# Performance work log

Hardware: AMD Instinct MI355X
Metric: run time of the kernel (lower is better)

The kernel has to match this reference:

```python
import jax, jax.numpy as jnp
import numpy as np

HEADS = 8
DIM = 64      # dim
DH = 64       # dim_head
DK = 24       # dim_k (== dim_head_k * heads, required by reshape in forward)
DHK = 3       # dim_head_k (also conv groups)


def setup_inputs() -> dict:
    key = jax.random.key(0)
    ks = jax.random.split(key, 10)
    b, h, w = 4, 128, 128
    return {
        "x_in": jax.random.normal(ks[0], (b, h, w, DIM), jnp.float32),
        "illu_fea_trans": jax.random.normal(ks[1], (b, h, w, DIM), jnp.float32),
        "illu_map_trans": jax.random.normal(ks[2], (b, h, w, DK), jnp.float32),
        # Linear weights stored as [in, out] (torch stores [out, in]; math y = x @ W_in_out)
        "Wq": jax.random.normal(ks[3], (DIM, HEADS * DH), jnp.float32) * 0.05,
        "Wk": jax.random.normal(ks[4], (DK, HEADS * DHK), jnp.float32) * 0.05,
        "Wv": jax.random.normal(ks[5], (DIM, HEADS * DH), jnp.float32) * 0.05,
        "rescale": jnp.ones((HEADS, 1, 1), jnp.float32),
        "Wp": jax.random.normal(ks[6], (HEADS * DHK, DK), jnp.float32) * 0.05,
        "bp": jax.random.normal(ks[7], (DK,), jnp.float32) * 0.05,
        # grouped conv weights, OIHW: [out=24, in/groups=8, 3, 3]
        "conv1_w": jax.random.normal(ks[8], (DK, DK // DHK, 3, 3), jnp.float32) * 0.05,
        "conv2_w": jax.random.normal(ks[9], (DK, DK // DHK, 3, 3), jnp.float32) * 0.05,
    }


def _gconv(x_nchw, w_oihw):
    return jax.lax.conv_general_dilated(
        x_nchw, w_oihw, window_strides=(1, 1), padding='SAME',
        feature_group_count=DHK,
        dimension_numbers=('NCHW', 'OIHW', 'NCHW'))


def reference(x_in, illu_fea_trans, illu_map_trans, Wq, Wk, Wv, rescale, Wp, bp, conv1_w, conv2_w):
    b, h, w, c = x_in.shape
    n = h * w
    # projections
    q = (x_in.reshape(b, n, c) @ Wq).reshape(b, n, HEADS, DH)
    k_inp = illu_map_trans.reshape(b, n, DK) @ Wk            # [b, n, heads*dhk]
    v = (illu_fea_trans.reshape(b, n, c) @ Wv).reshape(b, n, HEADS, DH)
    kh = k_inp.reshape(b, n, HEADS, DHK)
    q = q / (DIM ** 0.5)  # note: scaled by sqrt(dim), not sqrt(dim_head)
    # channel-wise cross-attention: attn over channel dims, contracting tokens n
    attn = jnp.einsum('bnhk,bnhd->bhkd', kh, q) * rescale[None]  # [b, heads, dhk, dh]
    attn = jax.nn.softmax(attn, axis=-1)
    out = jnp.einsum('bhkd,bnhd->bnkh', attn, v)             # [b, n, dhk, heads]
    out = out.reshape(b, n, DHK * HEADS) @ Wp + bp           # proj
    out = out.reshape(b, h, w, DK)
    # positional branch: two grouped 3x3 convs with exact GELU on k_inp
    kx = k_inp.reshape(b, h, w, DK).transpose(0, 3, 1, 2)    # NCHW
    y = _gconv(kx, conv1_w)
    y = jax.nn.gelu(y, approximate=False)
    y = _gconv(y, conv2_w)
    return out + y.transpose(0, 2, 3, 1)
```

## Files before the change

### kernel.cpp

```cpp
#include <hip/hip_runtime.h>
#include <math.h>

#define HEADS 8
#define DIM   64
#define DK    24
#define DHK   3
#define BB    4
#define HH    128
#define WW    128
#define NN    (HH*WW)
#define QSCALE 0.125f

__global__ __launch_bounds__(256) void s_reduce_kproj(
    const float* __restrict__ imap,
    const float* __restrict__ x,
    const float* __restrict__ Wk,
    float* __restrict__ k_inp,
    float* __restrict__ Sp_part)
{
    __shared__ float lds[4*1536];
    const int tid = threadIdx.x;
    const int blk = blockIdx.x;
    const int b = blk >> 7, chunk = blk & 127;
    const int w = tid >> 6, lane = tid & 63;
    const int cq = lane & 15;
    const int ig = lane >> 4;

    const long tokB = (long)b * NN + chunk * 128;
    const long tok0 = tokB + w * 32;
    const float* xp = x    + tok0 * 64 + cq * 4;
    const float* mp = imap + tok0 * 24 + ig * 6;

    float acc[6][4];
    #pragma unroll
    for (int r = 0; r < 6; ++r)
        #pragma unroll
        for (int q = 0; q < 4; ++q) acc[r][q] = 0.f;

    for (int t = 0; t < 32; ++t) {
        float4 xv = *(const float4*)(xp + t * 64);
        float2 m0 = *(const float2*)(mp + t * 24);
        float2 m1 = *(const float2*)(mp + t * 24 + 2);
        float2 m2 = *(const float2*)(mp + t * 24 + 4);
        float mm[6] = {m0.x, m0.y, m1.x, m1.y, m2.x, m2.y};
        #pragma unroll
        for (int r = 0; r < 6; ++r) {
            acc[r][0] += mm[r] * xv.x;
            acc[r][1] += mm[r] * xv.y;
            acc[r][2] += mm[r] * xv.z;
            acc[r][3] += mm[r] * xv.w;
        }
    }

    float* pp = lds + w * 1536;
    #pragma unroll
    for (int r = 0; r < 6; ++r) {
        float4 v = {acc[r][0], acc[r][1], acc[r][2], acc[r][3]};
        *(float4*)(pp + (ig * 6 + r) * 64 + cq * 4) = v;
    }
    __syncthreads();

    for (int e = tid; e < 1536; e += 256)
        Sp_part[(long)blk * 1536 + e] =
            lds[e] + lds[1536 + e] + lds[3072 + e] + lds[4608 + e];

    float kv[24];
    if (tid < 128) {
        const float4* m4 = (const float4*)(imap + (tokB + tid) * 24);
        float m[24];
        #pragma unroll
        for (int i = 0; i < 6; ++i) {
            float4 v = m4[i];
            m[4*i+0]=v.x; m[4*i+1]=v.y; m[4*i+2]=v.z; m[4*i+3]=v.w;
        }
        #pragma unroll
        for (int j = 0; j < 24; ++j) kv[j] = 0.f;
        for (int i = 0; i < 24; ++i) {
            float mi = m[i];
            #pragma unroll
            for (int j = 0; j < 24; ++j) kv[j] += mi * Wk[i * 24 + j];
        }
    }
    __syncthreads();
    if (tid < 128) {
        #pragma unroll
        for (int j = 0; j < 24; ++j) lds[tid * 25 + j] = kv[j];
    }
    __syncthreads();
    for (int e = tid; e < 128 * 24; e += 256)
        k_inp[tokB * 24 + e] = lds[(e / 24) * 25 + (e % 24)];
}

__global__ __launch_bounds__(256) void sp_reduce(
    const float* __restrict__ Sp_part, float* __restrict__ Sp)
{
    const int blk = blockIdx.x;
    const int b = blk / 6, eb = blk % 6;
    const int e = eb * 256 + threadIdx.x;
    const float* p = Sp_part + (long)b * 128 * 1536 + e;
    float s0 = 0.f, s1 = 0.f, s2 = 0.f, s3 = 0.f;
    for (int c = 0; c < 128; c += 4) {
        s0 += p[(long)(c + 0) * 1536];
        s1 += p[(long)(c + 1) * 1536];
        s2 += p[(long)(c + 2) * 1536];
        s3 += p[(long)(c + 3) * 1536];
    }
    Sp[b * 1536 + e] = (s0 + s1) + (s2 + s3);
}

__global__ __launch_bounds__(256) void attn_p(
    const float* __restrict__ Sp,
    const float* __restrict__ Wk,
    const float* __restrict__ Wq,
    const float* __restrict__ Wv,
    const float* __restrict__ rescale,
    const float* __restrict__ Wp,
    float* __restrict__ Pt)
{
    __shared__ float Sp_l[1536];
    __shared__ float S_l[1536];
    __shared__ float att[1536];
    __shared__ float M_l[1536];

    const int b = blockIdx.x, tid = threadIdx.x;

    for (int i = tid; i < 1536; i += 256) Sp_l[i] = Sp[b * 1536 + i];
    __syncthreads();

    for (int q = tid; q < 1536; q += 256) {
        int c = q & 63, j = q >> 6;
        float s = 0.f;
        #pragma unroll
        for (int i = 0; i < 24; ++i) s += Wk[i * 24 + j] * Sp_l[i * 64 + c];
        S_l[q] = s;
    }
    __syncthreads();

    for (int q = tid; q < 1536; q += 256) {
        int d = q & 63, ch = q >> 6;
        int h = ch / 3;
        const float* wq = Wq + h * 64 + d;
        const float* sr = S_l + ch * 64;
        float s = 0.f;
        for (int cc = 0; cc < 64; ++cc) s += sr[cc] * wq[cc * 512];
        att[q] = s * QSCALE * rescale[h];
    }
    __syncthreads();

    if (tid < 24) {
        float* row = att + tid * 64;
        float mx = row[0];
        for (int d = 1; d < 64; ++d) mx = fmaxf(mx, row[d]);
        float sum = 0.f;
        for (int d = 0; d < 64; ++d) { float e = expf(row[d] - mx); row[d] = e; sum += e; }
        float inv = 1.f / sum;
        for (int d = 0; d < 64; ++d) row[d] *= inv;
    }
    __syncthreads();

    for (int q = tid; q < 1536; q += 256) {
        int c = q & 63, ch = q >> 6;
        int h = ch / 3;
        const float* wv = Wv + c * 512 + h * 64;
        const float* ar = att + ch * 64;
        float s = 0.f;
        for (int d = 0; d < 64; ++d) s += ar[d] * wv[d];
        M_l[ch * 64 + c] = s;
    }
    __syncthreads();

    for (int q = tid; q < 1536; q += 256) {
        int c = q & 63, jo = q >> 6;
        float s = 0.f;
        #pragma unroll
        for (int k = 0; k < 3; ++k)
            #pragma unroll
            for (int h = 0; h < 8; ++h)
                s += M_l[(h * 3 + k) * 64 + c] * Wp[(k * 8 + h) * 24 + jo];
        Pt[b * 1536 + q] = s;
    }
}

#define CONV_PROLOG(CWPTR)                                                    \
    const int tid = threadIdx.x;                                              \
    const int o = tid % 24, jj = tid / 24;                                    \
    const int blk = blockIdx.x;                                               \
    const int b = blk >> 8, ti = (blk >> 4) & 15, tj = blk & 15;              \
    const int i0 = ti * 8, j0 = tj * 8;                                       \
    const int g = o >> 3;                                                     \
    float wr[8][9];                                                           \
    {                                                                         \
        const float4* wp = (const float4*)((CWPTR) + o * 72);                 \
        _Pragma("unroll")                                                     \
        for (int t = 0; t < 18; ++t) ((float4*)wr)[t] = wp[t];                \
    }                                                                         \
    const int gj0 = j0 + jj - 1;                                              \
    const bool cok0 = gj0 >= 0;                                               \
    const bool cok2 = (j0 + jj + 1) < WW;

#define LOADROW(IN, GI, SLOT)                                                 \
    {                                                                         \
        const int gi_ = (GI);                                                 \
        const bool rok_ = (gi_ >= 0) & (gi_ < HH);                            \
        const float* rp_ = (IN) + (long)b * NN * 24 + g * 8                   \
                         + ((long)gi_ * WW + gj0) * 24;                       \
        float4 z_ = {0.f,0.f,0.f,0.f};                                        \
        float4 a0_=z_, a1_=z_, b0_=z_, b1_=z_, c0_=z_, c1_=z_;                \
        if (rok_ & cok0) { a0_ = *(const float4*)(rp_);                       \
                           a1_ = *(const float4*)(rp_ + 4); }                 \
        if (rok_)        { b0_ = *(const float4*)(rp_ + 24);                  \
                           b1_ = *(const float4*)(rp_ + 28); }                \
        if (rok_ & cok2) { c0_ = *(const float4*)(rp_ + 48);                  \
                           c1_ = *(const float4*)(rp_ + 52); }                \
        *(float4*)&win[SLOT][0][0] = a0_; *(float4*)&win[SLOT][0][4] = a1_;   \
        *(float4*)&win[SLOT][1][0] = b0_; *(float4*)&win[SLOT][1][4] = b1_;   \
        *(float4*)&win[SLOT][2][0] = c0_; *(float4*)&win[SLOT][2][4] = c1_;   \
    }

__global__ __launch_bounds__(192, 2) void conv1_gelu(
    const float* __restrict__ kin, const float* __restrict__ cw,
    float* __restrict__ y1)
{
    CONV_PROLOG(cw)
    float win[3][3][8];
    LOADROW(kin, i0 - 1, 0)
    LOADROW(kin, i0,     1)
    #pragma unroll
    for (int ii = 0; ii < 8; ++ii) {
        LOADROW(kin, i0 + ii + 1, (ii + 2) % 3)
        float s = 0.f;
        #pragma unroll
        for (int di = 0; di < 3; ++di) {
            const int slot = (ii + di) % 3;
            #pragma unroll
            for (int dj = 0; dj < 3; ++dj)
                #pragma unroll
                for (int ic = 0; ic < 8; ++ic)
                    s += win[slot][dj][ic] * wr[ic][di * 3 + dj];
        }
        s = 0.5f * s * (1.f + erff(s * 0.70710678f));
        y1[((long)((b * HH + i0 + ii) * WW + j0)) * 24 + tid] = s;
    }
}

__global__ __launch_bounds__(192, 2) void conv2_proj(
    const float* __restrict__ y1, const float* __restrict__ fea,
    const float* __restrict__ cw2, const float* __restrict__ Pt,
    const float* __restrict__ bp, float* __restrict__ outp)
{
    CONV_PROLOG(cw2)

    float acc[8];
    {
        const float bo = bp[o];
        #pragma unroll
        for (int ii = 0; ii < 8; ++ii) acc[ii] = bo;
        const float* PtRow = Pt + b * 1536 + o * 64;
        const float* feaB = fea + (((long)(b * HH + i0)) * WW + (j0 + jj)) * 64;
        for (int cq = 0; cq < 16; ++cq) {
            float4 p = *(const float4*)(PtRow + cq * 4);
            #pragma unroll
            for (int ii = 0; ii < 8; ++ii) {
                float4 f = *(const float4*)(feaB + (long)ii * WW * 64 + cq * 4);
                acc[ii] += f.x * p.x + f.y * p.y + f.z * p.z + f.w * p.w;
            }
        }
    }

    float win[3][3][8];
    LOADROW(y1, i0 - 1, 0)
    LOADROW(y1, i0,     1)
    #pragma unroll
    for (int ii = 0; ii < 8; ++ii) {
        LOADROW(y1, i0 + ii + 1, (ii + 2) % 3)
        float s = 0.f;
        #pragma unroll
        for (int di = 0; di < 3; ++di) {
            const int slot = (ii + di) % 3;
            #pragma unroll
            for (int dj = 0; dj < 3; ++dj)
                #pragma unroll
                for (int ic = 0; ic < 8; ++ic)
                    s += win[slot][dj][ic] * wr[ic][di * 3 + dj];
        }
        outp[((long)((b * HH + i0 + ii) * WW + j0)) * 24 + tid] = acc[ii] + s;
    }
}

extern "C" void kernel_launch(void* const* d_in, const int* in_sizes, int n_in,
                              void* d_out, int out_size, void* d_ws, size_t ws_size,
                              hipStream_t stream) {
    const float* x_in    = (const float*)d_in[0];
    const float* fea     = (const float*)d_in[1];
    const float* imap    = (const float*)d_in[2];
    const float* Wq      = (const float*)d_in[3];
    const float* Wk      = (const float*)d_in[4];
    const float* Wv      = (const float*)d_in[5];
    const float* rescale = (const float*)d_in[6];
    const float* Wp      = (const float*)d_in[7];
    const float* bp      = (const float*)d_in[8];
    const float* c1w     = (const float*)d_in[9];
    const float* c2w     = (const float*)d_in[10];
    float* out = (float*)d_out;

    float* ws      = (float*)d_ws;
    float* k_inp   = ws;
    float* y1      = ws + 1572864;
    float* Sp_part = ws + 3145728;
    float* Sp      = ws + 3932160;
    float* Pt      = ws + 3938304;

    s_reduce_kproj<<<512, 256, 0, stream>>>(imap, x_in, Wk, k_inp, Sp_part);
    sp_reduce<<<24, 256, 0, stream>>>(Sp_part, Sp);
    attn_p<<<4, 256, 0, stream>>>(Sp, Wk, Wq, Wv, rescale, Wp, Pt);
    conv1_gelu<<<BB * 256, 192, 0, stream>>>(k_inp, c1w, y1);
    conv2_proj<<<BB * 256, 192, 0, stream>>>(y1, fea, c2w, Pt, bp, out);
}
```

Baseline: 178.8 us.

## Fuse k projection into conv1 via LDS halo tile and fold Sp reduction into attention

Computes the Wk projection of illu_map directly inside the first conv kernel for a 10x10 halo tile in shared memory, eliminating the k_inp global buffer write and reread. The separate Sp partial-reduction kernel is removed and its summation moved into the 4-block attention kernel. This cuts one launch and global traffic, at the cost of redundant halo projection work and a less parallel reduction running on only four blocks.

```diff
diff --git a/kernel.cpp b/kernel.cpp
--- a/kernel.cpp
+++ b/kernel.cpp
@@ -11,14 +11,12 @@
 #define NN    (HH*WW)
 #define QSCALE 0.125f
 
-__global__ __launch_bounds__(256) void s_reduce_kproj(
+__global__ __launch_bounds__(256) void s_reduce(
     const float* __restrict__ imap,
     const float* __restrict__ x,
-    const float* __restrict__ Wk,
-    float* __restrict__ k_inp,
     float* __restrict__ Sp_part)
 {
-    __shared__ float lds[4*1536];
+    __shared__ float part[4*1536];
     const int tid = threadIdx.x;
     const int blk = blockIdx.x;
     const int b = blk >> 7, chunk = blk & 127;
@@ -26,8 +24,7 @@
     const int cq = lane & 15;
     const int ig = lane >> 4;
 
-    const long tokB = (long)b * NN + chunk * 128;
-    const long tok0 = tokB + w * 32;
+    const long tok0 = (long)b * NN + chunk * 128 + w * 32;
     const float* xp = x    + tok0 * 64 + cq * 4;
     const float* mp = imap + tok0 * 24 + ig * 6;
 
@@ -52,7 +49,7 @@
         }
     }
 
-    float* pp = lds + w * 1536;
+    float* pp = part + w * 1536;
     #pragma unroll
     for (int r = 0; r < 6; ++r) {
         float4 v = {acc[r][0], acc[r][1], acc[r][2], acc[r][3]};
@@ -62,54 +59,11 @@
 
     for (int e = tid; e < 1536; e += 256)
         Sp_part[(long)blk * 1536 + e] =
-            lds[e] + lds[1536 + e] + lds[3072 + e] + lds[4608 + e];
-
-    float kv[24];
-    if (tid < 128) {
-        const float4* m4 = (const float4*)(imap + (tokB + tid) * 24);
-        float m[24];
-        #pragma unroll
-        for (int i = 0; i < 6; ++i) {
-            float4 v = m4[i];
-            m[4*i+0]=v.x; m[4*i+1]=v.y; m[4*i+2]=v.z; m[4*i+3]=v.w;
-        }
-        #pragma unroll
-        for (int j = 0; j < 24; ++j) kv[j] = 0.f;
-        for (int i = 0; i < 24; ++i) {
-            float mi = m[i];
-            #pragma unroll
-            for (int j = 0; j < 24; ++j) kv[j] += mi * Wk[i * 24 + j];
-        }
-    }
-    __syncthreads();
-    if (tid < 128) {
-        #pragma unroll
-        for (int j = 0; j < 24; ++j) lds[tid * 25 + j] = kv[j];
-    }
-    __syncthreads();
-    for (int e = tid; e < 128 * 24; e += 256)
-        k_inp[tokB * 24 + e] = lds[(e / 24) * 25 + (e % 24)];
-}
-
-__global__ __launch_bounds__(256) void sp_reduce(
-    const float* __restrict__ Sp_part, float* __restrict__ Sp)
-{
-    const int blk = blockIdx.x;
-    const int b = blk / 6, eb = blk % 6;
-    const int e = eb * 256 + threadIdx.x;
-    const float* p = Sp_part + (long)b * 128 * 1536 + e;
-    float s0 = 0.f, s1 = 0.f, s2 = 0.f, s3 = 0.f;
-    for (int c = 0; c < 128; c += 4) {
-        s0 += p[(long)(c + 0) * 1536];
-        s1 += p[(long)(c + 1) * 1536];
-        s2 += p[(long)(c + 2) * 1536];
-        s3 += p[(long)(c + 3) * 1536];
-    }
-    Sp[b * 1536 + e] = (s0 + s1) + (s2 + s3);
-}
-
-__global__ __launch_bounds__(256) void attn_p(
-    const float* __restrict__ Sp,
+            part[e] + part[1536 + e] + part[3072 + e] + part[4608 + e];
+}
+
+__global__ __launch_bounds__(256) void attn_fused(
+    const float* __restrict__ Sp_part,
     const float* __restrict__ Wk,
     const float* __restrict__ Wq,
     const float* __restrict__ Wv,
@@ -124,7 +78,17 @@
 
     const int b = blockIdx.x, tid = threadIdx.x;
 
-    for (int i = tid; i < 1536; i += 256) Sp_l[i] = Sp[b * 1536 + i];
+    {
+        float s[6] = {0.f, 0.f, 0.f, 0.f, 0.f, 0.f};
+        const float* p = Sp_part + (long)b * 128 * 1536;
+        for (int c = 0; c < 128; ++c) {
+            #pragma unroll
+            for (int k = 0; k < 6; ++k)
+                s[k] += p[(long)c * 1536 + tid + 256 * k];
+        }
+        #pragma unroll
+        for (int k = 0; k < 6; ++k) Sp_l[tid + 256 * k] = s[k];
+    }
     __syncthreads();
 
     for (int q = tid; q < 1536; q += 256) {
@@ -181,28 +145,130 @@
     }
 }
 
-#define CONV_PROLOG(CWPTR)                                                    \
-    const int tid = threadIdx.x;                                              \
-    const int o = tid % 24, jj = tid / 24;                                    \
-    const int blk = blockIdx.x;                                               \
-    const int b = blk >> 8, ti = (blk >> 4) & 15, tj = blk & 15;              \
-    const int i0 = ti * 8, j0 = tj * 8;                                       \
-    const int g = o >> 3;                                                     \
-    float wr[8][9];                                                           \
+__global__ __launch_bounds__(192, 2) void conv1_kproj_gelu(
+    const float* __restrict__ imap, const float* __restrict__ Wk,
+    const float* __restrict__ cw, float* __restrict__ y1)
+{
+    __shared__ __align__(16) float kbuf[100 * 28];
+
+    const int tid = threadIdx.x;
+    const int blk = blockIdx.x;
+    const int b = blk >> 8, ti = (blk >> 4) & 15, tj = blk & 15;
+    const int i0 = ti * 8, j0 = tj * 8;
+
+    if (tid < 100) {
+        const int pi = tid / 10, pj = tid % 10;
+        const int gi = i0 + pi - 1, gj = j0 + pj - 1;
+        float kv[24];
+        #pragma unroll
+        for (int j = 0; j < 24; ++j) kv[j] = 0.f;
+        if (gi >= 0 && gi < HH && gj >= 0 && gj < WW) {
+            const float4* m4 = (const float4*)(imap + (((long)b * HH + gi) * WW + gj) * 24);
+            float m[24];
+            #pragma unroll
+            for (int i = 0; i < 6; ++i) {
+                float4 v = m4[i];
+                m[4*i+0]=v.x; m[4*i+1]=v.y; m[4*i+2]=v.z; m[4*i+3]=v.w;
+            }
+            for (int i = 0; i < 24; ++i) {
+                float mi = m[i];
+                #pragma unroll
+                for (int j = 0; j < 24; ++j) kv[j] += mi * Wk[i * 24 + j];
+            }
+        }
+        #pragma unroll
+        for (int j = 0; j < 24; ++j) kbuf[tid * 28 + j] = kv[j];
+    }
+    __syncthreads();
+
+    const int o = tid % 24, jj = tid / 24;
+    const int g = o >> 3;
+
+    float wr[8][9];
+    {
+        const float4* wp = (const float4*)(cw + o * 72);
+        #pragma unroll
+        for (int t = 0; t < 18; ++t) ((float4*)wr)[t] = wp[t];
+    }
+
+    float win[3][3][8];
+    #define LROW(R, SLOT)                                                     \
     {                                                                         \
-        const float4* wp = (const float4*)((CWPTR) + o * 72);                 \
-        _Pragma("unroll")                                                     \
-        for (int t = 0; t < 18; ++t) ((float4*)wr)[t] = wp[t];                \
-    }                                                                         \
-    const int gj0 = j0 + jj - 1;                                              \
-    const bool cok0 = gj0 >= 0;                                               \
+        const float* rp_ = kbuf + ((R) * 10 + jj) * 28 + g * 8;               \
+        *(float4*)&win[SLOT][0][0] = *(const float4*)(rp_);                   \
+        *(float4*)&win[SLOT][0][4] = *(const float4*)(rp_ + 4);               \
+        *(float4*)&win[SLOT][1][0] = *(const float4*)(rp_ + 28);              \
+        *(float4*)&win[SLOT][1][4] = *(const float4*)(rp_ + 32);              \
+        *(float4*)&win[SLOT][2][0] = *(const float4*)(rp_ + 56);              \
+        *(float4*)&win[SLOT][2][4] = *(const float4*)(rp_ + 60);              \
+    }
+
+    LROW(0, 0)
+    LROW(1, 1)
+    #pragma unroll
+    for (int ii = 0; ii < 8; ++ii) {
+        LROW(ii + 2, (ii + 2) % 3)
+        float s = 0.f;
+        #pragma unroll
+        for (int di = 0; di < 3; ++di) {
+            const int slot = (ii + di) % 3;
+            #pragma unroll
+            for (int dj = 0; dj < 3; ++dj)
+                #pragma unroll
+                for (int ic = 0; ic < 8; ++ic)
+                    s += win[slot][dj][ic] * wr[ic][di * 3 + dj];
+        }
+        s = 0.5f * s * (1.f + erff(s * 0.70710678f));
+        y1[((long)((b * HH + i0 + ii) * WW + j0)) * 24 + tid] = s;
+    }
+    #undef LROW
+}
+
+__global__ __launch_bounds__(192, 2) void conv2_proj(
+    const float* __restrict__ y1, const float* __restrict__ fea,
+    const float* __restrict__ cw2, const float* __restrict__ Pt,
+    const float* __restrict__ bp, float* __restrict__ outp)
+{
+    const int tid = threadIdx.x;
+    const int o = tid % 24, jj = tid / 24;
+    const int blk = blockIdx.x;
+    const int b = blk >> 8, ti = (blk >> 4) & 15, tj = blk & 15;
+    const int i0 = ti * 8, j0 = tj * 8;
+    const int g = o >> 3;
+
+    float wr[8][9];
+    {
+        const float4* wp = (const float4*)(cw2 + o * 72);
+        #pragma unroll
+        for (int t = 0; t < 18; ++t) ((float4*)wr)[t] = wp[t];
+    }
+    const int gj0 = j0 + jj - 1;
+    const bool cok0 = gj0 >= 0;
     const bool cok2 = (j0 + jj + 1) < WW;
 
-#define LOADROW(IN, GI, SLOT)                                                 \
+    float acc[8];
+    {
+        const float bo = bp[o];
+        #pragma unroll
+        for (int ii = 0; ii < 8; ++ii) acc[ii] = bo;
+        const float* PtRow = Pt + b * 1536 + o * 64;
+        const float* feaB = fea + (((long)(b * HH + i0)) * WW + (j0 + jj)) * 64;
+        for (int cq = 0; cq < 16; ++cq) {
+            float4 p = *(const float4*)(PtRow + cq * 4);
+            #pragma unroll
+            for (int ii = 0; ii < 8; ++ii) {
+                float4 f = *(const float4*)(feaB + (long)ii * WW * 64 + cq * 4);
+                acc[ii] += f.x * p.x + f.y * p.y + f.z * p.z + f.w * p.w;
+            }
+        }
+    }
+
+    float win[3][3][8];
+    #define LOADROW(GI, SLOT)                                                 \
     {                                                                         \
         const int gi_ = (GI);                                                 \
         const bool rok_ = (gi_ >= 0) & (gi_ < HH);                            \
-        const float* rp_ = (IN) + (long)b * NN * 24 + g * 8                   \
+        const float* rp_ = y1 + (long)b * NN * 24 + g * 8                     \
                          + ((long)gi_ * WW + gj0) * 24;                       \
         float4 z_ = {0.f,0.f,0.f,0.f};                                        \
         float4 a0_=z_, a1_=z_, b0_=z_, b1_=z_, c0_=z_, c1_=z_;                \
@@ -217,17 +283,11 @@
         *(float4*)&win[SLOT][2][0] = c0_; *(float4*)&win[SLOT][2][4] = c1_;   \
     }
 
-__global__ __launch_bounds__(192, 2) void conv1_gelu(
-    const float* __restrict__ kin, const float* __restrict__ cw,
-    float* __restrict__ y1)
-{
-    CONV_PROLOG(cw)
-    float win[3][3][8];
-    LOADROW(kin, i0 - 1, 0)
-    LOADROW(kin, i0,     1)
+    LOADROW(i0 - 1, 0)
+    LOADROW(i0,     1)
     #pragma unroll
     for (int ii = 0; ii < 8; ++ii) {
-        LOADROW(kin, i0 + ii + 1, (ii + 2) % 3)
+        LOADROW(i0 + ii + 1, (ii + 2) % 3)
         float s = 0.f;
         #pragma unroll
         for (int di = 0; di < 3; ++di) {
@@ -238,53 +298,9 @@
                 for (int ic = 0; ic < 8; ++ic)
                     s += win[slot][dj][ic] * wr[ic][di * 3 + dj];
         }
-        s = 0.5f * s * (1.f + erff(s * 0.70710678f));
-        y1[((long)((b * HH + i0 + ii) * WW + j0)) * 24 + tid] = s;
-    }
-}
-
-__global__ __launch_bounds__(192, 2) void conv2_proj(
-    const float* __restrict__ y1, const float* __restrict__ fea,
-    const float* __restrict__ cw2, const float* __restrict__ Pt,
-    const float* __restrict__ bp, float* __restrict__ outp)
-{
-    CONV_PROLOG(cw2)
-
-    float acc[8];
-    {
-        const float bo = bp[o];
-        #pragma unroll
-        for (int ii = 0; ii < 8; ++ii) acc[ii] = bo;
-        const float* PtRow = Pt + b * 1536 + o * 64;
-        const float* feaB = fea + (((long)(b * HH + i0)) * WW + (j0 + jj)) * 64;
-        for (int cq = 0; cq < 16; ++cq) {
-            float4 p = *(const float4*)(PtRow + cq * 4);
-            #pragma unroll
-            for (int ii = 0; ii < 8; ++ii) {
-                float4 f = *(const float4*)(feaB + (long)ii * WW * 64 + cq * 4);
-                acc[ii] += f.x * p.x + f.y * p.y + f.z * p.z + f.w * p.w;
-            }
-        }
-    }
-
-    float win[3][3][8];
-    LOADROW(y1, i0 - 1, 0)
-    LOADROW(y1, i0,     1)
-    #pragma unroll
-    for (int ii = 0; ii < 8; ++ii) {
-        LOADROW(y1, i0 + ii + 1, (ii + 2) % 3)
-        float s = 0.f;
-        #pragma unroll
-        for (int di = 0; di < 3; ++di) {
-            const int slot = (ii + di) % 3;
-            #pragma unroll
-            for (int dj = 0; dj < 3; ++dj)
-                #pragma unroll
-                for (int ic = 0; ic < 8; ++ic)
-                    s += win[slot][dj][ic] * wr[ic][di * 3 + dj];
-        }
         outp[((long)((b * HH + i0 + ii) * WW + j0)) * 24 + tid] = acc[ii] + s;
     }
+    #undef LOADROW
 }
 
 extern "C" void kernel_launch(void* const* d_in, const int* in_sizes, int n_in,
@@ -304,15 +320,12 @@
     float* out = (float*)d_out;
 
     float* ws      = (float*)d_ws;
-    float* k_inp   = ws;
-    float* y1      = ws + 1572864;
-    float* Sp_part = ws + 3145728;
-    float* Sp      = ws + 3932160;
-    float* Pt      = ws + 3938304;
-
-    s_reduce_kproj<<<512, 256, 0, stream>>>(imap, x_in, Wk, k_inp, Sp_part);
-    sp_reduce<<<24, 256, 0, stream>>>(Sp_part, Sp);
-    attn_p<<<4, 256, 0, stream>>>(Sp, Wk, Wq, Wv, rescale, Wp, Pt);
-    conv1_gelu<<<BB * 256, 192, 0, stream>>>(k_inp, c1w, y1);
+    float* y1      = ws;
+    float* Sp_part = ws + 1572864;
+    float* Pt      = ws + 2359296;
+
+    s_reduce<<<512, 256, 0, stream>>>(imap, x_in, Sp_part);
+    attn_fused<<<4, 256, 0, stream>>>(Sp_part, Wk, Wq, Wv, rescale, Wp, Pt);
+    conv1_kproj_gelu<<<BB * 256, 192, 0, stream>>>(imap, Wk, c1w, y1);
     conv2_proj<<<BB * 256, 192, 0, stream>>>(y1, fea, c2w, Pt, bp, out);
 }
```

Result: slower. 190.3 us (+6.5%).
